# Performance work log

Measured on AMD Instinct MI355X. Metric: run time of the kernel, lower is better.

Reference implementation:

```python
import jax, jax.numpy as jnp
import numpy as np

# GPT-2 decoder (mlm=False path of the Keras GPT module), no past/KV-cache,
# no explicit mask -> causal mask, dropout disabled (training=False).
N_HEAD = 12
NINF = -10000.0  # Attention.ninf
EPS = 1e-6


def layer_norm(x, g, b):
    m = jnp.mean(x, axis=-1, keepdims=True)
    v = jnp.mean(jnp.square(x - m), axis=-1, keepdims=True)
    return (x - m) / jnp.sqrt(v + EPS) * g + b


def gelu(x):
    # 0.5*x*(1+erf(x/sqrt(2))) as in gelu_activating
    return 0.5 * x * (1.0 + jax.lax.erf(x * np.float32(1.0 / np.sqrt(2.0))))


def setup_inputs() -> dict:
    key = jax.random.key(0)
    B, S, D, L, V, CTX = 4, 512, 768, 12, 50257, 1024
    F = 4 * D
    ks = jax.random.split(key, 10)
    init = lambda k, shape: (jax.random.normal(k, shape, jnp.float32) * 0.02)
    return {
        "x": jax.random.randint(ks[0], (B, S), 0, V),
        "emb": init(ks[1], (V, D)),        # wte (tied output projection)
        "posemb": init(ks[2], (CTX, D)),   # wpe
        "ln1_g": jnp.ones((L, D)), "ln1_b": jnp.zeros((L, D)),
        "wqkv": init(ks[3], (L, D, 3 * D)), "bqkv": jnp.zeros((L, 3 * D)),
        "wo": init(ks[4], (L, D, D)), "bo": jnp.zeros((L, D)),
        "ln2_g": jnp.ones((L, D)), "ln2_b": jnp.zeros((L, D)),
        "wfc": init(ks[5], (L, D, F)), "bfc": jnp.zeros((L, F)),
        "wproj": init(ks[6], (L, F, D)), "bproj": jnp.zeros((L, D)),
        "lnf_g": jnp.ones((D,)), "lnf_b": jnp.zeros((D,)),
    }


def reference(x, emb, posemb, ln1_g, ln1_b, wqkv, bqkv, wo, bo,
              ln2_g, ln2_b, wfc, bfc, wproj, bproj, lnf_g, lnf_b):
    B, S = x.shape
    L, D, _ = wqkv.shape
    H = N_HEAD
    hd = D // H
    scale = np.float32(1.0 / np.sqrt(hd))

    # Embedding (mlm=False): token + positional, no layernorm
    h = emb[x] + posemb[:S]  # [B,S,D]

    # causal mask: positions j > i get NINF (m1 = range(q)[:,None] < range(k)-k+q)
    mask = (jnp.arange(S)[:, None] < jnp.arange(S)[None, :]).astype(jnp.float32) * NINF

    for i in range(L):
        # pre-norm attention
        qkv = layer_norm(h, ln1_g[i], ln1_b[i]) @ wqkv[i] + bqkv[i]  # [B,S,3D]
        q, k, v = jnp.split(qkv, 3, axis=-1)
        q = q.reshape(B, S, H, hd).transpose(0, 2, 1, 3)  # [B,H,S,hd]
        k = k.reshape(B, S, H, hd).transpose(0, 2, 1, 3)
        v = v.reshape(B, S, H, hd).transpose(0, 2, 1, 3)
        scores = jnp.einsum('bhqd,bhkd->bhqk', q, k) * scale + mask
        a = jax.nn.softmax(scores, axis=-1)  # [B,H,S,S]
        o = jnp.einsum('bhqk,bhkd->bhqd', a, v)
        o = o.transpose(0, 2, 1, 3).reshape(B, S, D)
        h = h + (o @ wo[i] + bo[i])  # residual
        # pre-norm MLP
        m = layer_norm(h, ln2_g[i], ln2_b[i])
        h = h + (gelu(m @ wfc[i] + bfc[i]) @ wproj[i] + bproj[i])

    hidden = layer_norm(h, lnf_g, lnf_b)          # model/lnorm_f
    logits = hidden @ emb.T                        # tied embedding projection
    probs = jax.nn.softmax(logits, axis=-1)        # softmax=True
    return (probs, hidden)
```

## Files before the change

kernel.cpp:

```cpp
#include <hip/hip_runtime.h>
#include <hip/hip_bf16.h>

typedef __bf16 bf16_t;
typedef bf16_t bf16x8 __attribute__((ext_vector_type(8)));
typedef float  f32x4  __attribute__((ext_vector_type(4)));

__device__ __forceinline__ void gload16(const void* g, void* l) {
    __builtin_amdgcn_global_load_lds(
        (const __attribute__((address_space(1))) unsigned int*)g,
        (__attribute__((address_space(3))) unsigned int*)l, 16, 0, 0);
}

__device__ __forceinline__ void drain_and_barrier() {
    __builtin_amdgcn_sched_barrier(0);
    asm volatile("s_waitcnt vmcnt(0)" ::: "memory");
    __builtin_amdgcn_s_barrier();
    __builtin_amdgcn_sched_barrier(0);
}

__global__ void embed_kernel(const int* __restrict__ x,
                             const float* __restrict__ emb,
                             const float* __restrict__ pos,
                             float* __restrict__ h,
                             int S, int D, int total)
{
    int i = blockIdx.x * blockDim.x + threadIdx.x;
    if (i >= total) return;
    int d  = i % D;
    int bs = i / D;
    int s  = bs % S;
    h[i] = emb[(long long)x[bs] * D + d] + pos[(long long)s * D + d];
}

__global__ void convert_bf16(const float* __restrict__ in, bf16_t* __restrict__ out, int n4)
{
    int i = blockIdx.x * blockDim.x + threadIdx.x;
    for (; i < n4; i += gridDim.x * blockDim.x) {
        float4 v = ((const float4*)in)[i];
        bf16_t* o = out + (size_t)i * 4;
        o[0] = (bf16_t)v.x; o[1] = (bf16_t)v.y; o[2] = (bf16_t)v.z; o[3] = (bf16_t)v.w;
    }
}

__global__ __launch_bounds__(256) void transpose_to_bf16(
    const float* __restrict__ in, bf16_t* __restrict__ out, int K, int N)
{
    const float* ip = in  + (size_t)blockIdx.z * K * N;
    bf16_t*      op = out + (size_t)blockIdx.z * K * N;
    __shared__ float t[32][33];
    const int n0 = blockIdx.x * 32, k0 = blockIdx.y * 32;
    const int tx = threadIdx.x, ty = threadIdx.y;
#pragma unroll
    for (int u = 0; u < 4; ++u)
        t[ty + u * 8][tx] = ip[(size_t)(k0 + ty + u * 8) * N + (n0 + tx)];
    __syncthreads();
#pragma unroll
    for (int u = 0; u < 4; ++u)
        op[(size_t)(n0 + ty + u * 8) * K + (k0 + tx)] = (bf16_t)t[tx][ty + u * 8];
}

__global__ __launch_bounds__(256) void layernorm_dual(
    const float* __restrict__ X, const float* __restrict__ g,
    const float* __restrict__ b, bf16_t* __restrict__ Yb,
    float* __restrict__ Yf, int D)
{
    const int row = blockIdx.x;
    const float* xr = X + (long long)row * D;
    const int tid = threadIdx.x;

    float vals[3];
    float s = 0.0f;
#pragma unroll
    for (int u = 0; u < 3; ++u) { vals[u] = xr[tid + u * 256]; s += vals[u]; }

    __shared__ float red[256];
    red[tid] = s;
    __syncthreads();
    for (int off = 128; off > 0; off >>= 1) {
        if (tid < off) red[tid] += red[tid + off];
        __syncthreads();
    }
    const float mean = red[0] / (float)D;
    __syncthreads();

    float vs = 0.0f;
#pragma unroll
    for (int u = 0; u < 3; ++u) { float d = vals[u] - mean; vs += d * d; }
    red[tid] = vs;
    __syncthreads();
    for (int off = 128; off > 0; off >>= 1) {
        if (tid < off) red[tid] += red[tid + off];
        __syncthreads();
    }
    const float var  = red[0] / (float)D;
    const float rstd = rsqrtf(var + 1e-6f);

#pragma unroll
    for (int u = 0; u < 3; ++u) {
        const int c = tid + u * 256;
        const float y = (vals[u] - mean) * rstd * g[c] + b[c];
        Yb[(long long)row * D + c] = (bf16_t)y;
        if (Yf) Yf[(long long)row * D + c] = y;
    }
}

__global__ __launch_bounds__(256) void flash_attn(
    const bf16_t* __restrict__ qkv, bf16_t* __restrict__ o)
{
    constexpr int S = 512, TD = 2304, D = 768, H = 12;
    const int qt = blockIdx.x;
    const int z  = blockIdx.y;
    const int bb = z / H, hh = z - bb * H;
    const int tid = threadIdx.x, lane = tid & 63, w = tid >> 6;
    const int fr = lane & 15, g = lane >> 4, sub = g * 8;

    __shared__ bf16_t kS[2][4096];
    __shared__ bf16_t vS[2][4096];
    __shared__ bf16_t pS[4][16 * 72];

    bf16x8 qf[2];
    const bf16_t* qbase = qkv + (size_t)(bb * S + qt * 64 + w * 16) * TD + hh * 64;
#pragma unroll
    for (int ks = 0; ks < 2; ++ks) {
        bf16x8 v = *(const bf16x8*)&qbase[(size_t)fr * TD + ks * 32 + sub];
#pragma unroll
        for (int j = 0; j < 8; ++j) v[j] = v[j] * (bf16_t)0.125f;
        qf[ks] = v;
    }

    f32x4 oacc[4];
    float mrun[4], lrun[4];
#pragma unroll
    for (int r = 0; r < 4; ++r) { mrun[r] = -3.0e38f; lrun[r] = 0.0f; }
#pragma unroll
    for (int n = 0; n < 4; ++n) oacc[n] = (f32x4){0.f, 0.f, 0.f, 0.f};

    int qr[4];
#pragma unroll
    for (int r = 0; r < 4; ++r) qr[r] = qt * 64 + w * 16 + g * 4 + r;

    const int srow8  = lane >> 3;
    const int schunk = (lane & 7) ^ (srow8 & 7);

    const bf16_t* kGbase = qkv + (size_t)(bb * S) * TD + D + hh * 64;
    const bf16_t* vGbase = qkv + (size_t)(bb * S) * TD + 2 * D + hh * 64;
    const int nkv = qt + 1;

    bf16x8 vreg[2];

#define STAGE_ISSUE(buf, t)                                                     \
    {                                                                           \
        _Pragma("unroll")                                                       \
        for (int it = 0; it < 2; ++it) {                                        \
            const int row = it * 32 + w * 8 + srow8;                            \
            gload16(kGbase + (size_t)((t) * 64 + row) * TD + schunk * 8,        \
                    &kS[buf][it * 2048 + w * 512]);                             \
        }                                                                       \
        _Pragma("unroll")                                                       \
        for (int it = 0; it < 2; ++it) {                                        \
            const int dch = w * 2 + it;                                         \
            vreg[it] = *(const bf16x8*)&vGbase[(size_t)((t) * 64 + lane) * TD + dch * 8]; \
        }                                                                       \
    }
#define STAGE_WRITE(buf)                                                        \
    {                                                                           \
        _Pragma("unroll")                                                       \
        for (int it = 0; it < 2; ++it) {                                        \
            const int dch = w * 2 + it;                                         \
            _Pragma("unroll")                                                   \
            for (int j = 0; j < 8; ++j) {                                       \
                const int d = dch * 8 + j;                                      \
                vS[buf][d * 64 + (((lane >> 3) ^ j) << 3) + (lane & 7)] = vreg[it][j]; \
            }                                                                   \
        }                                                                       \
    }

    STAGE_ISSUE(0, 0);
    STAGE_WRITE(0);
    __syncthreads();

    int cur = 0;
    for (int t = 0; t < nkv; ++t) {
        if (t + 1 < nkv) STAGE_ISSUE(cur ^ 1, t + 1);

        f32x4 sacc[4];
#pragma unroll
        for (int n = 0; n < 4; ++n) sacc[n] = (f32x4){0.f, 0.f, 0.f, 0.f};
#pragma unroll
        for (int ks = 0; ks < 2; ++ks) {
            bf16x8 bK[4];
#pragma unroll
            for (int n = 0; n < 4; ++n) {
                const int rw = n * 16 + fr;
                const int c  = ks * 4 + g;
                bK[n] = *(const bf16x8*)&kS[cur][rw * 64 + ((c ^ (rw & 7)) << 3)];
            }
#pragma unroll
            for (int n = 0; n < 4; ++n)
                sacc[n] = __builtin_amdgcn_mfma_f32_16x16x32_bf16(
                    qf[ks], bK[n], sacc[n], 0, 0, 0);
        }

        if (t == qt) {
#pragma unroll
            for (int n = 0; n < 4; ++n) {
                const int key = t * 64 + n * 16 + fr;
#pragma unroll
                for (int r = 0; r < 4; ++r)
                    if (key > qr[r]) sacc[n][r] = -3.0e38f;
            }
        }

        float sf[4], rs[4];
#pragma unroll
        for (int r = 0; r < 4; ++r) {
            float v = fmaxf(fmaxf(sacc[0][r], sacc[1][r]),
                            fmaxf(sacc[2][r], sacc[3][r]));
#pragma unroll
            for (int off = 1; off < 16; off <<= 1)
                v = fmaxf(v, __shfl_xor(v, off));
            const float mn = fmaxf(mrun[r], v);
            sf[r] = __expf(mrun[r] - mn);
            mrun[r] = mn;
            lrun[r] *= sf[r];
        }
#pragma unroll
        for (int n = 0; n < 4; ++n)
#pragma unroll
            for (int r = 0; r < 4; ++r)
                oacc[n][r] *= sf[r];
#pragma unroll
        for (int r = 0; r < 4; ++r) rs[r] = 0.0f;
#pragma unroll
        for (int n = 0; n < 4; ++n)
#pragma unroll
            for (int r = 0; r < 4; ++r) {
                const float p = __expf(sacc[n][r] - mrun[r]);
                sacc[n][r] = p;
                rs[r] += p;
            }
#pragma unroll
        for (int r = 0; r < 4; ++r) {
            float v = rs[r];
#pragma unroll
            for (int off = 1; off < 16; off <<= 1) v += __shfl_xor(v, off);
            lrun[r] += v;
        }

        bf16_t* pw = pS[w];
#pragma unroll
        for (int n = 0; n < 4; ++n)
#pragma unroll
            for (int r = 0; r < 4; ++r)
                pw[(g * 4 + r) * 72 + n * 16 + fr] = (bf16_t)sacc[n][r];

#pragma unroll
        for (int ks = 0; ks < 2; ++ks) {
            bf16x8 pa, vb[4];
            pa = *(const bf16x8*)&pw[fr * 72 + ks * 32 + sub];
#pragma unroll
            for (int n = 0; n < 4; ++n) {
                const int rw = n * 16 + fr;
                const int c  = ks * 4 + g;
                vb[n] = *(const bf16x8*)&vS[cur][rw * 64 + ((c ^ (rw & 7)) << 3)];
            }
#pragma unroll
            for (int n = 0; n < 4; ++n)
                oacc[n] = __builtin_amdgcn_mfma_f32_16x16x32_bf16(
                    pa, vb[n], oacc[n], 0, 0, 0);
        }

        if (t + 1 < nkv) STAGE_WRITE(cur ^ 1);
        __syncthreads();
        cur ^= 1;
    }
#undef STAGE_ISSUE
#undef STAGE_WRITE

    bf16_t* obase = o + (size_t)(bb * S + qt * 64 + w * 16) * D + hh * 64;
#pragma unroll
    for (int r = 0; r < 4; ++r) {
        const float inv = 1.0f / lrun[r];
#pragma unroll
        for (int n = 0; n < 4; ++n)
            obase[(size_t)(g * 4 + r) * D + n * 16 + fr] =
                (bf16_t)(oacc[n][r] * inv);
    }
}

__global__ __launch_bounds__(256) void softmax_vocab(
    const bf16_t* __restrict__ logits, float* __restrict__ probs, int V, int Vp)
{
    const int tid = threadIdx.x;
    const bf16_t* lr = logits + (size_t)blockIdx.x * Vp;
    float* pr = probs + (size_t)blockIdx.x * V;
    const int n8 = V >> 3;

    float m = -3.0e38f, s = 0.0f;
    for (int c8 = tid; c8 < n8; c8 += 256) {
        const bf16x8 v = *(const bf16x8*)(lr + (size_t)c8 * 8);
        float f[8], lm = -3.0e38f;
#pragma unroll
        for (int j = 0; j < 8; ++j) { f[j] = (float)v[j]; lm = fmaxf(lm, f[j]); }
        if (lm > m) { s *= __expf(m - lm); m = lm; }
#pragma unroll
        for (int j = 0; j < 8; ++j) s += __expf(f[j] - m);
    }
    for (int c = n8 * 8 + tid; c < V; c += 256) {
        const float f = (float)lr[c];
        if (f > m) { s *= __expf(m - f); m = f; }
        s += __expf(f - m);
    }

    __shared__ float mS[256], sS[256];
    mS[tid] = m; sS[tid] = s;
    __syncthreads();
    for (int off = 128; off > 0; off >>= 1) {
        if (tid < off) {
            const float m1 = mS[tid], m2 = mS[tid + off];
            const float M_ = fmaxf(m1, m2);
            sS[tid] = sS[tid] * __expf(m1 - M_) + sS[tid + off] * __expf(m2 - M_);
            mS[tid] = M_;
        }
        __syncthreads();
    }
    const float M_  = mS[0];
    const float inv = 1.0f / sS[0];

    for (int c8 = tid; c8 < n8; c8 += 256) {
        const bf16x8 v = *(const bf16x8*)(lr + (size_t)c8 * 8);
#pragma unroll
        for (int j = 0; j < 8; ++j)
            pr[(size_t)c8 * 8 + j] = __expf((float)v[j] - M_) * inv;
    }
    for (int c = n8 * 8 + tid; c < V; c += 256)
        pr[c] = __expf((float)lr[c] - M_) * inv;
}

template<bool ADD, bool GELU_, bool OUTBF>
__device__ __forceinline__ void gemm_body(
    const bf16_t* __restrict__ A, const bf16_t* __restrict__ Bw,
    const float* __restrict__ bias, void* __restrict__ Cv,
    int M, int N, int K, int lda, int ldb, int ldc)
{
    constexpr int BUF = 12288;
    __shared__ bf16_t lds[2 * BUF];

    const int tid  = threadIdx.x;
    const int lane = tid & 63;
    const int w    = tid >> 6;
    const int row0 = blockIdx.x * 128;
    const int col0 = blockIdx.y * 64;

    const int row8 = lane >> 3;
    const int sch  = (lane & 7) ^ row8;
    const int fr   = lane & 15;
    const int g    = lane >> 4;

    const int aRowB = row0 + w * 32;
    const int bRowB = col0 + w * 16;

    f32x4 acc[2][4];
#pragma unroll
    for (int m = 0; m < 2; ++m)
#pragma unroll
        for (int n = 0; n < 4; ++n)
            acc[m][n] = (f32x4){0.f, 0.f, 0.f, 0.f};

    auto STAGE = [&](int buf, int k0) {
        bf16_t* lb = lds + buf * BUF;
#pragma unroll
        for (int it = 0; it < 4; ++it) {
            const int ar = aRowB + it * 8 + row8;
            gload16(A + (size_t)ar * lda + k0 + sch * 8, lb + w * 2048 + it * 512);
        }
#pragma unroll
        for (int it = 0; it < 2; ++it) {
            int br = bRowB + it * 8 + row8;
            if (br >= N) br = 0;
            gload16(Bw + (size_t)br * ldb + k0 + sch * 8,
                    lb + 8192 + w * 1024 + it * 512);
        }
    };

    auto COMPUTE = [&](int buf) {
        bf16_t* lb = lds + buf * BUF;
#pragma unroll
        for (int ks = 0; ks < 2; ++ks) {
            bf16x8 af[2], bfr[4];
            const int cs = ks * 4 + g;
#pragma unroll
            for (int m = 0; m < 2; ++m) {
                const int row = w * 32 + m * 16 + fr;
                af[m] = *(const bf16x8*)&lb[row * 64 + ((cs ^ (fr & 7)) << 3)];
            }
#pragma unroll
            for (int n = 0; n < 4; ++n) {
                const int row = n * 16 + fr;
                bfr[n] = *(const bf16x8*)&lb[8192 + row * 64 + ((cs ^ (fr & 7)) << 3)];
            }
#pragma unroll
            for (int m = 0; m < 2; ++m)
#pragma unroll
                for (int n = 0; n < 4; ++n)
                    acc[m][n] = __builtin_amdgcn_mfma_f32_16x16x32_bf16(
                        af[m], bfr[n], acc[m][n], 0, 0, 0);
        }
    };

    const int nt = K >> 6;
    STAGE(0, 0);
    drain_and_barrier();
    int cur = 0;
    for (int t = 0; t < nt; ++t) {
        if (t + 1 < nt) STAGE(cur ^ 1, (t + 1) << 6);
        COMPUTE(cur);
        drain_and_barrier();
        cur ^= 1;
    }

    const int rBase = row0 + w * 32 + g * 4;
    const int cBase = col0 + fr;
    float bv[4];
#pragma unroll
    for (int n = 0; n < 4; ++n) {
        const int c = cBase + n * 16;
        bv[n] = (bias && c < N) ? bias[c] : 0.0f;
    }
#pragma unroll
    for (int m = 0; m < 2; ++m) {
#pragma unroll
        for (int r = 0; r < 4; ++r) {
            const int rr = rBase + m * 16 + r;
#pragma unroll
            for (int n = 0; n < 4; ++n) {
                const int c = cBase + n * 16;
                if (c >= N) continue;
                float v = acc[m][n][r] + bv[n];
                if (GELU_) v = 0.5f * v * (1.0f + erff(v * 0.70710678118654752f));
                if (OUTBF) {
                    ((bf16_t*)Cv)[(size_t)rr * ldc + c] = (bf16_t)v;
                } else {
                    float* Cf = (float*)Cv;
                    const size_t idx = (size_t)rr * ldc + c;
                    if (ADD) v += Cf[idx];
                    Cf[idx] = v;
                }
            }
        }
    }
}

__global__ __launch_bounds__(256) void k_gemm_qkv(
    const bf16_t* A, const bf16_t* B, const float* bias, void* C,
    int M, int N, int K, int lda, int ldb, int ldc)
{ gemm_body<false, false, true>(A, B, bias, C, M, N, K, lda, ldb, ldc); }

__global__ __launch_bounds__(256) void k_gemm_fc(
    const bf16_t* A, const bf16_t* B, const float* bias, void* C,
    int M, int N, int K, int lda, int ldb, int ldc)
{ gemm_body<false, true, true>(A, B, bias, C, M, N, K, lda, ldb, ldc); }

__global__ __launch_bounds__(256) void k_gemm_small(
    const bf16_t* __restrict__ A, const bf16_t* __restrict__ Bw,
    const float* __restrict__ bias, float* __restrict__ C,
    int M, int N, int K, int lda, int ldb, int ldc)
{
    constexpr int BUF = 8192;
    __shared__ bf16_t lds[2 * BUF];

    const int tid  = threadIdx.x;
    const int lane = tid & 63;
    const int w    = tid >> 6;
    const int row0 = blockIdx.x * 64;
    const int col0 = blockIdx.y * 64;

    const int row8 = lane >> 3;
    const int sch  = (lane & 7) ^ row8;
    const int fr   = lane & 15;
    const int g    = lane >> 4;

    f32x4 acc[4];
#pragma unroll
    for (int m = 0; m < 4; ++m) acc[m] = (f32x4){0.f, 0.f, 0.f, 0.f};

    auto STAGE = [&](int buf, int k0) {
        bf16_t* lb = lds + buf * BUF;
#pragma unroll
        for (int it = 0; it < 2; ++it) {
            const int ar = row0 + it * 32 + w * 8 + row8;
            gload16(A + (size_t)ar * lda + k0 + sch * 8,
                    lb + (it * 32 + w * 8) * 64);
            const int br = col0 + it * 32 + w * 8 + row8;
            gload16(Bw + (size_t)br * ldb + k0 + sch * 8,
                    lb + 4096 + (it * 32 + w * 8) * 64);
        }
    };

    auto COMPUTE = [&](int buf) {
        bf16_t* lb = lds + buf * BUF;
#pragma unroll
        for (int ks = 0; ks < 2; ++ks) {
            const int cs = ks * 4 + g;
            const int bRow = w * 16 + fr;
            bf16x8 bfr = *(const bf16x8*)&lb[4096 + bRow * 64 + ((cs ^ (fr & 7)) << 3)];
#pragma unroll
            for (int m = 0; m < 4; ++m) {
                const int row = m * 16 + fr;
                bf16x8 af = *(const bf16x8*)&lb[row * 64 + ((cs ^ (fr & 7)) << 3)];
                acc[m] = __builtin_amdgcn_mfma_f32_16x16x32_bf16(
                    af, bfr, acc[m], 0, 0, 0);
            }
        }
    };

    const int nt = K >> 6;
    STAGE(0, 0);
    drain_and_barrier();
    int cur = 0;
    for (int t = 0; t < nt; ++t) {
        if (t + 1 < nt) STAGE(cur ^ 1, (t + 1) << 6);
        COMPUTE(cur);
        drain_and_barrier();
        cur ^= 1;
    }

    const int c = col0 + w * 16 + fr;
    const float bv = bias ? bias[c] : 0.0f;
#pragma unroll
    for (int m = 0; m < 4; ++m) {
#pragma unroll
        for (int r = 0; r < 4; ++r) {
            const int rr = row0 + m * 16 + g * 4 + r;
            const size_t idx = (size_t)rr * ldc + c;
            C[idx] += acc[m][r] + bv;
        }
    }
}

__global__ __launch_bounds__(256) void k_gemm_head(
    const bf16_t* __restrict__ A, const bf16_t* __restrict__ Bw,
    bf16_t* __restrict__ C, int M, int N, int K, int lda, int ldb, int ldc)
{
    __shared__ bf16_t lds[16384];

    const int nwg = gridDim.x * gridDim.y;
    int flat = blockIdx.y * gridDim.x + blockIdx.x;
    {
        const int xcd = flat & 7, pos = flat >> 3;
        flat = xcd * (nwg >> 3) + pos;
    }
    const int bx = flat % gridDim.x;
    const int by = flat / gridDim.x;

    const int tid  = threadIdx.x;
    const int lane = tid & 63;
    const int w    = tid >> 6;
    const int wr   = w >> 1, wc = w & 1;
    const int row0 = bx * 128;
    const int col0 = by * 128;

    const int row8 = lane >> 3;
    const int sch  = (lane & 7) ^ row8;
    const int fr   = lane & 15;
    const int g    = lane >> 4;

    const int aRowB = row0 + w * 32;
    const int bRowB = col0 + w * 32;

    f32x4 acc[4][4];
#pragma unroll
    for (int m = 0; m < 4; ++m)
#pragma unroll
        for (int n = 0; n < 4; ++n)
            acc[m][n] = (f32x4){0.f, 0.f, 0.f, 0.f};

    for (int k0 = 0; k0 < K; k0 += 64) {
#pragma unroll
        for (int it = 0; it < 4; ++it) {
            const int ar = aRowB + it * 8 + row8;
            gload16(A + (size_t)ar * lda + k0 + sch * 8,
                    lds + w * 2048 + it * 512);
            int br = bRowB + it * 8 + row8;
            if (br >= N) br = 0;
            gload16(Bw + (size_t)br * ldb + k0 + sch * 8,
                    lds + 8192 + w * 2048 + it * 512);
        }
        __syncthreads();

#pragma unroll
        for (int ks = 0; ks < 2; ++ks) {
            bf16x8 af[4], bfr[4];
            const int cs = ks * 4 + g;
#pragma unroll
            for (int m = 0; m < 4; ++m) {
                const int row = wr * 64 + m * 16 + fr;
                af[m] = *(const bf16x8*)&lds[row * 64 + ((cs ^ (fr & 7)) << 3)];
            }
#pragma unroll
            for (int n = 0; n < 4; ++n) {
                const int row = wc * 64 + n * 16 + fr;
                bfr[n] = *(const bf16x8*)&lds[8192 + row * 64 + ((cs ^ (fr & 7)) << 3)];
            }
#pragma unroll
            for (int m = 0; m < 4; ++m)
#pragma unroll
                for (int n = 0; n < 4; ++n)
                    acc[m][n] = __builtin_amdgcn_mfma_f32_16x16x32_bf16(
                        af[m], bfr[n], acc[m][n], 0, 0, 0);
        }
        __syncthreads();
    }

    const int rBase = row0 + wr * 64 + g * 4;
    const int cBase = col0 + wc * 64 + fr;
#pragma unroll
    for (int n = 0; n < 4; ++n) {
        const int c = cBase + n * 16;
        if (c >= N) continue;
#pragma unroll
        for (int m = 0; m < 4; ++m)
#pragma unroll
            for (int r = 0; r < 4; ++r)
                C[(size_t)(rBase + m * 16 + r) * ldc + c] = (bf16_t)acc[m][n][r];
    }
}

extern "C" void kernel_launch(void* const* d_in, const int* in_sizes, int n_in,
                              void* d_out, int out_size, void* d_ws, size_t ws_size,
                              hipStream_t stream)
{
    constexpr int B = 4, S = 512, D = 768, L = 12, V = 50257, H = 12, F = 3072;
    constexpr int M  = B * S;
    constexpr int TD = 3 * D;
    constexpr int BH = B * H;
    constexpr int Vp = 50264;
    constexpr int NP = (V + 127) / 128;

    const int*   x    = (const int*)  d_in[0];
    const float* emb  = (const float*)d_in[1];
    const float* pos  = (const float*)d_in[2];
    const float* ln1g = (const float*)d_in[3];
    const float* ln1b = (const float*)d_in[4];
    const float* wqkv = (const float*)d_in[5];
    const float* bqkv = (const float*)d_in[6];
    const float* wo   = (const float*)d_in[7];
    const float* bo   = (const float*)d_in[8];
    const float* ln2g = (const float*)d_in[9];
    const float* ln2b = (const float*)d_in[10];
    const float* wfc  = (const float*)d_in[11];
    const float* bfc  = (const float*)d_in[12];
    const float* wpr  = (const float*)d_in[13];
    const float* bpr  = (const float*)d_in[14];
    const float* lnfg = (const float*)d_in[15];
    const float* lnfb = (const float*)d_in[16];

    float* probs  = (float*)d_out;
    float* hidden = probs + (size_t)M * V;

    char* wsb = (char*)d_ws;
    size_t off = 0;
    auto alloc = [&](size_t bytes) -> char* {
        char* p = wsb + off;
        off += (bytes + 255) & ~(size_t)255;
        return p;
    };
    bf16_t* hid_bf = (bf16_t*)alloc((size_t)M * D * 2);
    bf16_t* embB   = (bf16_t*)alloc((size_t)V * D * 2);
    const size_t trunk_start = off;
    float*  h      = (float*) alloc((size_t)M * D * 4);
    bf16_t* qkv_bf = (bf16_t*)alloc((size_t)M * TD * 2);
    bf16_t* xn_bf  = (bf16_t*)alloc((size_t)M * D * 2);
    bf16_t* o_bf   = (bf16_t*)alloc((size_t)M * D * 2);
    bf16_t* mid_bf = (bf16_t*)alloc((size_t)M * F * 2);
    bf16_t* wqkvT  = (bf16_t*)alloc((size_t)L * D * TD * 2);
    bf16_t* woT    = (bf16_t*)alloc((size_t)L * D * D * 2);
    bf16_t* wfcT   = (bf16_t*)alloc((size_t)L * D * F * 2);
    bf16_t* wprT   = (bf16_t*)alloc((size_t)L * F * D * 2);
    const size_t logits_bytes = (size_t)M * Vp * 2;
    if (off < trunk_start + logits_bytes) off = trunk_start + logits_bytes;
    bf16_t* logits = (bf16_t*)(wsb + trunk_start);

    convert_bf16<<<2048, 256, 0, stream>>>(emb, embB, (V * D) / 4);
    transpose_to_bf16<<<dim3(TD / 32, D / 32, L), dim3(32, 8), 0, stream>>>(wqkv, wqkvT, D, TD);
    transpose_to_bf16<<<dim3(D / 32,  D / 32, L), dim3(32, 8), 0, stream>>>(wo,   woT,   D, D);
    transpose_to_bf16<<<dim3(F / 32,  D / 32, L), dim3(32, 8), 0, stream>>>(wfc,  wfcT,  D, F);
    transpose_to_bf16<<<dim3(D / 32,  F / 32, L), dim3(32, 8), 0, stream>>>(wpr,  wprT,  F, D);

    embed_kernel<<<dim3((M * D + 255) / 256), 256, 0, stream>>>(x, emb, pos, h, S, D, M * D);

    for (int i = 0; i < L; ++i) {
        layernorm_dual<<<M, 256, 0, stream>>>(h, ln1g + (size_t)i * D, ln1b + (size_t)i * D,
                                              xn_bf, nullptr, D);

        k_gemm_qkv<<<dim3(M / 128, TD / 64), 256, 0, stream>>>(
            xn_bf, wqkvT + (size_t)i * D * TD, bqkv + (size_t)i * TD, qkv_bf,
            M, TD, D, D, D, TD);

        flash_attn<<<dim3(S / 64, BH), 256, 0, stream>>>(qkv_bf, o_bf);

        k_gemm_small<<<dim3(M / 64, D / 64), 256, 0, stream>>>(
            o_bf, woT + (size_t)i * D * D, bo + (size_t)i * D, h,
            M, D, D, D, D, D);

        layernorm_dual<<<M, 256, 0, stream>>>(h, ln2g + (size_t)i * D, ln2b + (size_t)i * D,
                                              xn_bf, nullptr, D);

        k_gemm_fc<<<dim3(M / 128, F / 64), 256, 0, stream>>>(
            xn_bf, wfcT + (size_t)i * D * F, bfc + (size_t)i * F, mid_bf,
            M, F, D, D, D, F);

        k_gemm_small<<<dim3(M / 64, D / 64), 256, 0, stream>>>(
            mid_bf, wprT + (size_t)i * F * D, bpr + (size_t)i * D, h,
            M, D, F, F, F, D);
    }

    layernorm_dual<<<M, 256, 0, stream>>>(h, lnfg, lnfb, hid_bf, hidden, D);

    k_gemm_head<<<dim3(M / 128, NP), 256, 0, stream>>>(
        hid_bf, embB, logits,
        M, V, D, D, D, Vp);

    softmax_vocab<<<M, 256, 0, stream>>>(logits, probs, V, Vp);
}
```

Baseline: 2.034 ms.

## Switch GEMMs to triple-buffered K=32 pipeline with partial vmcnt waits

Rewrites the qkv/fc, small, and head GEMM main loops to use three LDS buffers with 32-wide K tiles, prefetching two tiles ahead and waiting only on the oldest loads via partial s_waitcnt vmcnt counts instead of draining all loads each iteration. The LDS swizzle is changed to match 32-element rows, and the head GEMM gains prefetch it previously lacked. The aim is to keep global loads in flight across iterations and hide memory latency behind MFMA work. In exchange there are twice as many barriers per K, and the generic epilogue's N-bounds and null-bias checks are removed, so the code assumes exact tile multiples.

```diff
diff --git a/kernel.cpp b/kernel.cpp
--- a/kernel.cpp
+++ b/kernel.cpp
@@ -11,12 +11,10 @@
         (__attribute__((address_space(3))) unsigned int*)l, 16, 0, 0);
 }
 
-__device__ __forceinline__ void drain_and_barrier() {
-    __builtin_amdgcn_sched_barrier(0);
-    asm volatile("s_waitcnt vmcnt(0)" ::: "memory");
-    __builtin_amdgcn_s_barrier();
-    __builtin_amdgcn_sched_barrier(0);
-}
+#define WAITVM(n) do { \
+    asm volatile("s_waitcnt vmcnt(" #n ")" ::: "memory"); \
+    __builtin_amdgcn_sched_barrier(0); \
+} while (0)
 
 __global__ void embed_kernel(const int* __restrict__ x,
                              const float* __restrict__ emb,
@@ -337,14 +335,15 @@
         pr[c] = __expf((float)lr[c] - M_) * inv;
 }
 
-template<bool ADD, bool GELU_, bool OUTBF>
+
+template<bool GELU_>
 __device__ __forceinline__ void gemm_body(
     const bf16_t* __restrict__ A, const bf16_t* __restrict__ Bw,
-    const float* __restrict__ bias, void* __restrict__ Cv,
+    const float* __restrict__ bias, bf16_t* __restrict__ C,
     int M, int N, int K, int lda, int ldb, int ldc)
 {
-    constexpr int BUF = 12288;
-    __shared__ bf16_t lds[2 * BUF];
+    constexpr int BUF = 6144;
+    __shared__ bf16_t lds[3 * BUF];
 
     const int tid  = threadIdx.x;
     const int lane = tid & 63;
@@ -352,14 +351,11 @@
     const int row0 = blockIdx.x * 128;
     const int col0 = blockIdx.y * 64;
 
-    const int row8 = lane >> 3;
-    const int sch  = (lane & 7) ^ row8;
+    const int srow = lane >> 2;
+    const int sch  = (lane & 3) ^ (srow & 3);
     const int fr   = lane & 15;
     const int g    = lane >> 4;
 
-    const int aRowB = row0 + w * 32;
-    const int bRowB = col0 + w * 16;
-
     f32x4 acc[2][4];
 #pragma unroll
     for (int m = 0; m < 2; ++m)
@@ -367,66 +363,61 @@
         for (int n = 0; n < 4; ++n)
             acc[m][n] = (f32x4){0.f, 0.f, 0.f, 0.f};
 
-    auto STAGE = [&](int buf, int k0) {
+    auto STAGE = [&](int buf, int t) {
         bf16_t* lb = lds + buf * BUF;
-#pragma unroll
-        for (int it = 0; it < 4; ++it) {
-            const int ar = aRowB + it * 8 + row8;
-            gload16(A + (size_t)ar * lda + k0 + sch * 8, lb + w * 2048 + it * 512);
-        }
+        const int k0 = t << 5;
 #pragma unroll
         for (int it = 0; it < 2; ++it) {
-            int br = bRowB + it * 8 + row8;
-            if (br >= N) br = 0;
-            gload16(Bw + (size_t)br * ldb + k0 + sch * 8,
-                    lb + 8192 + w * 1024 + it * 512);
-        }
+            const int ar = row0 + w * 32 + it * 16 + srow;
+            gload16(A + (size_t)ar * lda + k0 + sch * 8,
+                    lb + (w * 32 + it * 16) * 32);
+        }
+        const int br = col0 + w * 16 + srow;
+        gload16(Bw + (size_t)br * ldb + k0 + sch * 8,
+                lb + 4096 + (w * 16) * 32);
     };
 
     auto COMPUTE = [&](int buf) {
         bf16_t* lb = lds + buf * BUF;
-#pragma unroll
-        for (int ks = 0; ks < 2; ++ks) {
-            bf16x8 af[2], bfr[4];
-            const int cs = ks * 4 + g;
-#pragma unroll
-            for (int m = 0; m < 2; ++m) {
-                const int row = w * 32 + m * 16 + fr;
-                af[m] = *(const bf16x8*)&lb[row * 64 + ((cs ^ (fr & 7)) << 3)];
-            }
-#pragma unroll
-            for (int n = 0; n < 4; ++n) {
-                const int row = n * 16 + fr;
-                bfr[n] = *(const bf16x8*)&lb[8192 + row * 64 + ((cs ^ (fr & 7)) << 3)];
-            }
-#pragma unroll
-            for (int m = 0; m < 2; ++m)
-#pragma unroll
-                for (int n = 0; n < 4; ++n)
-                    acc[m][n] = __builtin_amdgcn_mfma_f32_16x16x32_bf16(
-                        af[m], bfr[n], acc[m][n], 0, 0, 0);
-        }
+        bf16x8 af[2], bfr[4];
+#pragma unroll
+        for (int m = 0; m < 2; ++m) {
+            const int row = w * 32 + m * 16 + fr;
+            af[m] = *(const bf16x8*)&lb[row * 32 + ((g ^ (row & 3)) << 3)];
+        }
+#pragma unroll
+        for (int n = 0; n < 4; ++n) {
+            const int row = n * 16 + fr;
+            bfr[n] = *(const bf16x8*)&lb[4096 + row * 32 + ((g ^ (row & 3)) << 3)];
+        }
+#pragma unroll
+        for (int m = 0; m < 2; ++m)
+#pragma unroll
+            for (int n = 0; n < 4; ++n)
+                acc[m][n] = __builtin_amdgcn_mfma_f32_16x16x32_bf16(
+                    af[m], bfr[n], acc[m][n], 0, 0, 0);
     };
 
-    const int nt = K >> 6;
-    STAGE(0, 0);
-    drain_and_barrier();
-    int cur = 0;
+    const int nt = K >> 5;
+    STAGE(0, 0); STAGE(1, 1); STAGE(2, 2);
+    WAITVM(6);
+    __builtin_amdgcn_s_barrier();
+    int b0 = 0;
     for (int t = 0; t < nt; ++t) {
-        if (t + 1 < nt) STAGE(cur ^ 1, (t + 1) << 6);
-        COMPUTE(cur);
-        drain_and_barrier();
-        cur ^= 1;
+        COMPUTE(b0);
+        if (t + 1 < nt) {
+            if (t + 2 < nt) { WAITVM(3); } else { WAITVM(0); }
+        }
+        __builtin_amdgcn_s_barrier();
+        if (t + 3 < nt) STAGE(b0, t + 3);
+        b0 = (b0 == 2) ? 0 : b0 + 1;
     }
 
     const int rBase = row0 + w * 32 + g * 4;
     const int cBase = col0 + fr;
     float bv[4];
 #pragma unroll
-    for (int n = 0; n < 4; ++n) {
-        const int c = cBase + n * 16;
-        bv[n] = (bias && c < N) ? bias[c] : 0.0f;
-    }
+    for (int n = 0; n < 4; ++n) bv[n] = bias[cBase + n * 16];
 #pragma unroll
     for (int m = 0; m < 2; ++m) {
 #pragma unroll
@@ -434,40 +425,31 @@
             const int rr = rBase + m * 16 + r;
 #pragma unroll
             for (int n = 0; n < 4; ++n) {
-                const int c = cBase + n * 16;
-                if (c >= N) continue;
                 float v = acc[m][n][r] + bv[n];
                 if (GELU_) v = 0.5f * v * (1.0f + erff(v * 0.70710678118654752f));
-                if (OUTBF) {
-                    ((bf16_t*)Cv)[(size_t)rr * ldc + c] = (bf16_t)v;
-                } else {
-                    float* Cf = (float*)Cv;
-                    const size_t idx = (size_t)rr * ldc + c;
-                    if (ADD) v += Cf[idx];
-                    Cf[idx] = v;
-                }
+                C[(size_t)rr * ldc + cBase + n * 16] = (bf16_t)v;
             }
         }
     }
 }
 
 __global__ __launch_bounds__(256) void k_gemm_qkv(
-    const bf16_t* A, const bf16_t* B, const float* bias, void* C,
+    const bf16_t* A, const bf16_t* B, const float* bias, bf16_t* C,
     int M, int N, int K, int lda, int ldb, int ldc)
-{ gemm_body<false, false, true>(A, B, bias, C, M, N, K, lda, ldb, ldc); }
+{ gemm_body<false>(A, B, bias, C, M, N, K, lda, ldb, ldc); }
 
 __global__ __launch_bounds__(256) void k_gemm_fc(
-    const bf16_t* A, const bf16_t* B, const float* bias, void* C,
+    const bf16_t* A, const bf16_t* B, const float* bias, bf16_t* C,
     int M, int N, int K, int lda, int ldb, int ldc)
-{ gemm_body<false, true, true>(A, B, bias, C, M, N, K, lda, ldb, ldc); }
+{ gemm_body<true>(A, B, bias, C, M, N, K, lda, ldb, ldc); }
 
 __global__ __launch_bounds__(256) void k_gemm_small(
     const bf16_t* __restrict__ A, const bf16_t* __restrict__ Bw,
     const float* __restrict__ bias, float* __restrict__ C,
     int M, int N, int K, int lda, int ldb, int ldc)
 {
-    constexpr int BUF = 8192;
-    __shared__ bf16_t lds[2 * BUF];
+    constexpr int BUF = 4096;
+    __shared__ bf16_t lds[3 * BUF];
 
     const int tid  = threadIdx.x;
     const int lane = tid & 63;
@@ -475,8 +457,8 @@
     const int row0 = blockIdx.x * 64;
     const int col0 = blockIdx.y * 64;
 
-    const int row8 = lane >> 3;
-    const int sch  = (lane & 7) ^ row8;
+    const int srow = lane >> 2;
+    const int sch  = (lane & 3) ^ (srow & 3);
     const int fr   = lane & 15;
     const int g    = lane >> 4;
 
@@ -484,56 +466,50 @@
 #pragma unroll
     for (int m = 0; m < 4; ++m) acc[m] = (f32x4){0.f, 0.f, 0.f, 0.f};
 
-    auto STAGE = [&](int buf, int k0) {
+    auto STAGE = [&](int buf, int t) {
         bf16_t* lb = lds + buf * BUF;
-#pragma unroll
-        for (int it = 0; it < 2; ++it) {
-            const int ar = row0 + it * 32 + w * 8 + row8;
-            gload16(A + (size_t)ar * lda + k0 + sch * 8,
-                    lb + (it * 32 + w * 8) * 64);
-            const int br = col0 + it * 32 + w * 8 + row8;
-            gload16(Bw + (size_t)br * ldb + k0 + sch * 8,
-                    lb + 4096 + (it * 32 + w * 8) * 64);
-        }
+        const int k0 = t << 5;
+        const int ar = row0 + w * 16 + srow;
+        gload16(A + (size_t)ar * lda + k0 + sch * 8, lb + (w * 16) * 32);
+        const int br = col0 + w * 16 + srow;
+        gload16(Bw + (size_t)br * ldb + k0 + sch * 8, lb + 2048 + (w * 16) * 32);
     };
 
     auto COMPUTE = [&](int buf) {
         bf16_t* lb = lds + buf * BUF;
-#pragma unroll
-        for (int ks = 0; ks < 2; ++ks) {
-            const int cs = ks * 4 + g;
-            const int bRow = w * 16 + fr;
-            bf16x8 bfr = *(const bf16x8*)&lb[4096 + bRow * 64 + ((cs ^ (fr & 7)) << 3)];
-#pragma unroll
-            for (int m = 0; m < 4; ++m) {
-                const int row = m * 16 + fr;
-                bf16x8 af = *(const bf16x8*)&lb[row * 64 + ((cs ^ (fr & 7)) << 3)];
-                acc[m] = __builtin_amdgcn_mfma_f32_16x16x32_bf16(
-                    af, bfr, acc[m], 0, 0, 0);
-            }
+        const int bRow = w * 16 + fr;
+        bf16x8 bfr = *(const bf16x8*)&lb[2048 + bRow * 32 + ((g ^ (bRow & 3)) << 3)];
+#pragma unroll
+        for (int m = 0; m < 4; ++m) {
+            const int row = m * 16 + fr;
+            bf16x8 af = *(const bf16x8*)&lb[row * 32 + ((g ^ (row & 3)) << 3)];
+            acc[m] = __builtin_amdgcn_mfma_f32_16x16x32_bf16(af, bfr, acc[m], 0, 0, 0);
         }
     };
 
-    const int nt = K >> 6;
-    STAGE(0, 0);
-    drain_and_barrier();
-    int cur = 0;
+    const int nt = K >> 5;
+    STAGE(0, 0); STAGE(1, 1); STAGE(2, 2);
+    WAITVM(4);
+    __builtin_amdgcn_s_barrier();
+    int b0 = 0;
     for (int t = 0; t < nt; ++t) {
-        if (t + 1 < nt) STAGE(cur ^ 1, (t + 1) << 6);
-        COMPUTE(cur);
-        drain_and_barrier();
-        cur ^= 1;
+        COMPUTE(b0);
+        if (t + 1 < nt) {
+            if (t + 2 < nt) { WAITVM(2); } else { WAITVM(0); }
+        }
+        __builtin_amdgcn_s_barrier();
+        if (t + 3 < nt) STAGE(b0, t + 3);
+        b0 = (b0 == 2) ? 0 : b0 + 1;
     }
 
     const int c = col0 + w * 16 + fr;
-    const float bv = bias ? bias[c] : 0.0f;
+    const float bv = bias[c];
 #pragma unroll
     for (int m = 0; m < 4; ++m) {
 #pragma unroll
         for (int r = 0; r < 4; ++r) {
             const int rr = row0 + m * 16 + g * 4 + r;
-            const size_t idx = (size_t)rr * ldc + c;
-            C[idx] += acc[m][r] + bv;
+            C[(size_t)rr * ldc + c] += acc[m][r] + bv;
         }
     }
 }
@@ -542,7 +518,8 @@
     const bf16_t* __restrict__ A, const bf16_t* __restrict__ Bw,
     bf16_t* __restrict__ C, int M, int N, int K, int lda, int ldb, int ldc)
 {
-    __shared__ bf16_t lds[16384];
+    constexpr int BUF = 8192;
+    __shared__ bf16_t lds[3 * BUF];
 
     const int nwg = gridDim.x * gridDim.y;
     int flat = blockIdx.y * gridDim.x + blockIdx.x;
@@ -560,14 +537,11 @@
     const int row0 = bx * 128;
     const int col0 = by * 128;
 
-    const int row8 = lane >> 3;
-    const int sch  = (lane & 7) ^ row8;
+    const int srow = lane >> 2;
+    const int sch  = (lane & 3) ^ (srow & 3);
     const int fr   = lane & 15;
     const int g    = lane >> 4;
 
-    const int aRowB = row0 + w * 32;
-    const int bRowB = col0 + w * 32;
-
     f32x4 acc[4][4];
 #pragma unroll
     for (int m = 0; m < 4; ++m)
@@ -575,41 +549,55 @@
         for (int n = 0; n < 4; ++n)
             acc[m][n] = (f32x4){0.f, 0.f, 0.f, 0.f};
 
-    for (int k0 = 0; k0 < K; k0 += 64) {
-#pragma unroll
-        for (int it = 0; it < 4; ++it) {
-            const int ar = aRowB + it * 8 + row8;
+    auto STAGE = [&](int buf, int t) {
+        bf16_t* lb = lds + buf * BUF;
+        const int k0 = t << 5;
+#pragma unroll
+        for (int it = 0; it < 2; ++it) {
+            const int ar = row0 + w * 32 + it * 16 + srow;
             gload16(A + (size_t)ar * lda + k0 + sch * 8,
-                    lds + w * 2048 + it * 512);
-            int br = bRowB + it * 8 + row8;
+                    lb + (w * 32 + it * 16) * 32);
+            int br = col0 + w * 32 + it * 16 + srow;
             if (br >= N) br = 0;
             gload16(Bw + (size_t)br * ldb + k0 + sch * 8,
-                    lds + 8192 + w * 2048 + it * 512);
-        }
-        __syncthreads();
-
-#pragma unroll
-        for (int ks = 0; ks < 2; ++ks) {
-            bf16x8 af[4], bfr[4];
-            const int cs = ks * 4 + g;
-#pragma unroll
-            for (int m = 0; m < 4; ++m) {
-                const int row = wr * 64 + m * 16 + fr;
-                af[m] = *(const bf16x8*)&lds[row * 64 + ((cs ^ (fr & 7)) << 3)];
-            }
-#pragma unroll
-            for (int n = 0; n < 4; ++n) {
-                const int row = wc * 64 + n * 16 + fr;
-                bfr[n] = *(const bf16x8*)&lds[8192 + row * 64 + ((cs ^ (fr & 7)) << 3)];
-            }
-#pragma unroll
-            for (int m = 0; m < 4; ++m)
-#pragma unroll
-                for (int n = 0; n < 4; ++n)
-                    acc[m][n] = __builtin_amdgcn_mfma_f32_16x16x32_bf16(
-                        af[m], bfr[n], acc[m][n], 0, 0, 0);
-        }
-        __syncthreads();
+                    lb + 4096 + (w * 32 + it * 16) * 32);
+        }
+    };
+
+    auto COMPUTE = [&](int buf) {
+        bf16_t* lb = lds + buf * BUF;
+        bf16x8 af[4], bfr[4];
+#pragma unroll
+        for (int m = 0; m < 4; ++m) {
+            const int row = wr * 64 + m * 16 + fr;
+            af[m] = *(const bf16x8*)&lb[row * 32 + ((g ^ (row & 3)) << 3)];
+        }
+#pragma unroll
+        for (int n = 0; n < 4; ++n) {
+            const int row = wc * 64 + n * 16 + fr;
+            bfr[n] = *(const bf16x8*)&lb[4096 + row * 32 + ((g ^ (row & 3)) << 3)];
+        }
+#pragma unroll
+        for (int m = 0; m < 4; ++m)
+#pragma unroll
+            for (int n = 0; n < 4; ++n)
+                acc[m][n] = __builtin_amdgcn_mfma_f32_16x16x32_bf16(
+                    af[m], bfr[n], acc[m][n], 0, 0, 0);
+    };
+
+    const int nt = K >> 5;
+    STAGE(0, 0); STAGE(1, 1); STAGE(2, 2);
+    WAITVM(8);
+    __builtin_amdgcn_s_barrier();
+    int b0 = 0;
+    for (int t = 0; t < nt; ++t) {
+        COMPUTE(b0);
+        if (t + 1 < nt) {
+            if (t + 2 < nt) { WAITVM(4); } else { WAITVM(0); }
+        }
+        __builtin_amdgcn_s_barrier();
+        if (t + 3 < nt) STAGE(b0, t + 3);
+        b0 = (b0 == 2) ? 0 : b0 + 1;
     }
 
     const int rBase = row0 + wr * 64 + g * 4;
```

Result: slower. 2.108 ms (+3.7%).
